# Kernel tuning notes

Measured on AMD Instinct MI355X. Metric: run time of the kernel, lower is better.

Reference implementation:

```python
import jax, jax.numpy as jnp
import numpy as np

D_MODEL = 1024
NUM_HEADS = 16
D_K = D_MODEL // NUM_HEADS
THETA = 10000.0


def _rope(x, pos):
    # x: [B, H, S, D_K], pos: [S]
    angles = 1.0 / (THETA ** (jnp.arange(0, D_K, 2, dtype=jnp.float32) / D_K))  # [D_K/2]
    ang = pos.astype(jnp.float32)[:, None] * angles  # [S, D_K/2]
    cos = jnp.repeat(jnp.cos(ang), 2, axis=-1)  # [S, D_K]
    sin = jnp.repeat(jnp.sin(ang), 2, axis=-1)
    x2 = x.reshape(*x.shape[:-1], D_K // 2, 2)
    xr = jnp.stack([-x2[..., 1], x2[..., 0]], axis=-1).reshape(x.shape)
    return x * cos + xr * sin


def setup_inputs() -> dict:
    key = jax.random.key(0)
    ks = jax.random.split(key, 5)
    B, S = 2, 2048
    sd = np.sqrt(2.0 / (D_MODEL + D_MODEL))
    return {
        "x": jax.random.normal(ks[0], (B, S, D_MODEL), dtype=jnp.float32),
        "token_positions": jnp.arange(S, dtype=jnp.int32),
        "Wq": jax.random.normal(ks[1], (D_MODEL, D_MODEL), dtype=jnp.float32) * sd,
        "Wk": jax.random.normal(ks[2], (D_MODEL, D_MODEL), dtype=jnp.float32) * sd,
        "Wv": jax.random.normal(ks[3], (D_MODEL, D_MODEL), dtype=jnp.float32) * sd,
        "Wo": jax.random.normal(ks[4], (D_MODEL, D_MODEL), dtype=jnp.float32) * sd,
    }


def reference(x, token_positions, Wq, Wk, Wv, Wo):
    B, S, _ = x.shape

    def proj_heads(W):
        y = jnp.einsum('bsd,ed->bse', x, W)  # weight stored [d_out, d_in]
        return y.reshape(B, S, NUM_HEADS, D_K).transpose(0, 2, 1, 3)  # [B,H,S,Dk]

    q = _rope(proj_heads(Wq), token_positions)
    k = _rope(proj_heads(Wk), token_positions)
    v = proj_heads(Wv)

    scores = jnp.einsum('bhqd,bhkd->bhqk', q, k) / np.sqrt(D_K)  # [B,H,S,S]
    causal = jnp.tril(jnp.ones((S, S), dtype=bool))
    scores = jnp.where(causal, scores, -jnp.inf)
    attn = jax.nn.softmax(scores, axis=-1)
    out = jnp.einsum('bhqk,bhkd->bhqd', attn, v)  # [B,H,S,Dk]
    out = out.transpose(0, 2, 1, 3).reshape(B, S, D_MODEL)
    return jnp.einsum('bsd,ed->bse', out, Wo)
```

## Files before the change

### kernel.cpp

```cpp
#include <hip/hip_runtime.h>
#include <hip/hip_bf16.h>
#include <cstdint>
#include <cmath>

#define SEQ 2048
#define NH 16
#define DM 1024
#define BATCH 2

typedef short bf16x8 __attribute__((ext_vector_type(8)));
typedef float f32x4 __attribute__((ext_vector_type(4)));
typedef const void __attribute__((address_space(1)))* gas_t;
typedef void __attribute__((address_space(3)))* las_t;

#if __has_builtin(__builtin_amdgcn_exp2f)
#define EXP2(x) __builtin_amdgcn_exp2f(x)
#else
#define EXP2(x) __expf((x) * 0.6931471805599453f)
#endif

#define QSCALE 0.18033688011112042f

static __device__ __forceinline__ unsigned short f2bf(float f) {
    union { __hip_bfloat16 h; unsigned short u; } cv;
    cv.h = __float2bfloat16(f);
    return cv.u;
}
static __device__ __forceinline__ float bf2f(unsigned short u) {
    union { unsigned short u; __hip_bfloat16 h; } cv;
    cv.u = u;
    return __bfloat162float(cv.h);
}

static __device__ __forceinline__ void gload_lds16(const void* g, void* l) {
    __builtin_amdgcn_global_load_lds(
        reinterpret_cast<gas_t>(reinterpret_cast<uintptr_t>(g)),
        reinterpret_cast<las_t>(reinterpret_cast<uintptr_t>(l)),
        16, 0, 0);
}

__global__ __launch_bounds__(256) void cvt_all(
    const float* __restrict__ x,  const float* __restrict__ wq,
    const float* __restrict__ wk, const float* __restrict__ wv,
    const float* __restrict__ wo,
    unsigned short* __restrict__ xb, unsigned short* __restrict__ wqkv,
    unsigned short* __restrict__ wob) {
    int blk = blockIdx.x;
    const float* src; unsigned short* dst; int base;
    if (blk < 4096)      { src = x;  dst = xb;              base = blk; }
    else if (blk < 5120) { src = wq; dst = wqkv;            base = blk - 4096; }
    else if (blk < 6144) { src = wk; dst = wqkv + 1048576;  base = blk - 5120; }
    else if (blk < 7168) { src = wv; dst = wqkv + 2097152;  base = blk - 6144; }
    else                 { src = wo; dst = wob;             base = blk - 7168; }
    int i = base * 256 + threadIdx.x;
    float4 v = reinterpret_cast<const float4*>(src)[i];
    ushort4 o;
    o.x = f2bf(v.x); o.y = f2bf(v.y); o.z = f2bf(v.z); o.w = f2bf(v.w);
    reinterpret_cast<ushort4*>(dst)[i] = o;
}

template<int OUT_BF16>
__global__ __launch_bounds__(256) void gemm_bt(
    const unsigned short* __restrict__ A,
    const unsigned short* __restrict__ B,
    void* __restrict__ C, int M, int N, int K) {
    __shared__ unsigned short As[128 * 32];
    __shared__ unsigned short Bs[128 * 32];
    const int tid = threadIdx.x;
    const int lane = tid & 63, wid = tid >> 6;
    const int wr = wid >> 1, wc = wid & 1;
    const int ln15 = lane & 15, kq = lane >> 4;
    const int bm = blockIdx.y, bn = blockIdx.x;

    f32x4 acc[4][4] = {};
    const int nk = K >> 5;
    for (int kt = 0; kt < nk; ++kt) {
        #pragma unroll
        for (int i = 0; i < 2; ++i) {
            int c = i * 256 + tid;
            int row = c >> 2, k8 = (c & 3) << 3;
            size_t gofsA = (size_t)(bm * 128 + row) * K + kt * 32 + k8;
            size_t gofsB = (size_t)(bn * 128 + row) * K + kt * 32 + k8;
            unsigned ldsoff = (unsigned)(i * 256 + wid * 64) * 16;
            gload_lds16(A + gofsA, (char*)As + ldsoff);
            gload_lds16(B + gofsB, (char*)Bs + ldsoff);
        }
        __syncthreads();
        bf16x8 af[4], bf[4];
        #pragma unroll
        for (int m = 0; m < 4; ++m)
            af[m] = *reinterpret_cast<const bf16x8*>(&As[(wr * 64 + m * 16 + ln15) * 32 + kq * 8]);
        #pragma unroll
        for (int n = 0; n < 4; ++n)
            bf[n] = *reinterpret_cast<const bf16x8*>(&Bs[(wc * 64 + n * 16 + ln15) * 32 + kq * 8]);
        #pragma unroll
        for (int m = 0; m < 4; ++m)
            #pragma unroll
            for (int n = 0; n < 4; ++n)
                acc[m][n] = __builtin_amdgcn_mfma_f32_16x16x32_bf16(af[m], bf[n], acc[m][n], 0, 0, 0);
        __syncthreads();
    }
    #pragma unroll
    for (int m = 0; m < 4; ++m) {
        #pragma unroll
        for (int n = 0; n < 4; ++n) {
            int col = bn * 128 + wc * 64 + n * 16 + ln15;
            #pragma unroll
            for (int j = 0; j < 4; ++j) {
                int row = bm * 128 + wr * 64 + m * 16 + kq * 4 + j;
                if constexpr (OUT_BF16 != 0)
                    ((unsigned short*)C)[(size_t)row * N + col] = f2bf(acc[m][n][j]);
                else
                    ((float*)C)[(size_t)row * N + col] = acc[m][n][j];
            }
        }
    }
}

__global__ __launch_bounds__(512) void gemm256_bt(
    const unsigned short* __restrict__ A,
    const unsigned short* __restrict__ B,
    unsigned short* __restrict__ C, int M, int N, int K) {
    __shared__ unsigned short As[2][256 * 64];
    __shared__ unsigned short Bs[2][256 * 64];
    const int tid = threadIdx.x;
    const int lane = tid & 63, wid = tid >> 6;
    const int wm = wid >> 2, wn = wid & 3;
    const int ln15 = lane & 15, g = lane >> 4;
    const int bm = blockIdx.y, bn = blockIdx.x;

    const unsigned short* aSrc[4];
    const unsigned short* bSrc[4];
    #pragma unroll
    for (int p = 0; p < 4; ++p) {
        int c = tid + (p << 9);
        int row = c >> 3, slot = c & 7;
        aSrc[p] = A + (size_t)(bm * 256 + row) * K + ((slot ^ (row & 7)) << 3);
        bSrc[p] = B + (size_t)(bn * 256 + row) * K + ((slot ^ (row & 7)) << 3);
    }
    auto stage = [&](int kt, int buf) {
        #pragma unroll
        for (int p = 0; p < 4; ++p) {
            unsigned dst = (unsigned)(tid + (p << 9)) << 4;
            gload_lds16(aSrc[p] + kt * 64, (char*)As[buf] + dst);
            gload_lds16(bSrc[p] + kt * 64, (char*)Bs[buf] + dst);
        }
    };

    const unsigned ps0 = (unsigned)((g ^ (ln15 & 7)) << 4);
    const unsigned ps1 = (unsigned)(((4 + g) ^ (ln15 & 7)) << 4);
    const unsigned aBase = (unsigned)(wm * 128 + ln15) * 128;
    const unsigned bBase = (unsigned)(wn * 64 + ln15) * 128;

    f32x4 acc[8][4] = {};
    const int nkt = K >> 6;

    stage(0, 0);
    stage(1, 1);

    for (int t = 0; t < nkt; ++t) {
        const int cur = t & 1;
        if (t + 1 < nkt) {
            asm volatile("s_waitcnt vmcnt(8)" ::: "memory");
        } else {
            asm volatile("s_waitcnt vmcnt(0)" ::: "memory");
        }
        __builtin_amdgcn_s_barrier();

        const char* Ab = (const char*)As[cur];
        const char* Bb = (const char*)Bs[cur];
        bf16x8 bf[4][2];
        #pragma unroll
        for (int nf = 0; nf < 4; ++nf) {
            bf[nf][0] = *reinterpret_cast<const bf16x8*>(Bb + bBase + nf * 2048 + ps0);
            bf[nf][1] = *reinterpret_cast<const bf16x8*>(Bb + bBase + nf * 2048 + ps1);
        }
        __builtin_amdgcn_s_setprio(1);
        #pragma unroll
        for (int mf = 0; mf < 8; ++mf) {
            bf16x8 af0 = *reinterpret_cast<const bf16x8*>(Ab + aBase + mf * 2048 + ps0);
            bf16x8 af1 = *reinterpret_cast<const bf16x8*>(Ab + aBase + mf * 2048 + ps1);
            #pragma unroll
            for (int nf = 0; nf < 4; ++nf) {
                acc[mf][nf] = __builtin_amdgcn_mfma_f32_16x16x32_bf16(af0, bf[nf][0], acc[mf][nf], 0, 0, 0);
                acc[mf][nf] = __builtin_amdgcn_mfma_f32_16x16x32_bf16(af1, bf[nf][1], acc[mf][nf], 0, 0, 0);
            }
        }
        __builtin_amdgcn_s_setprio(0);
        asm volatile("s_waitcnt lgkmcnt(0)" ::: "memory");
        __builtin_amdgcn_s_barrier();
        if (t + 2 < nkt) stage(t + 2, cur);
    }

    #pragma unroll
    for (int mf = 0; mf < 8; ++mf) {
        #pragma unroll
        for (int nf = 0; nf < 4; ++nf) {
            int col = bn * 256 + wn * 64 + nf * 16 + ln15;
            #pragma unroll
            for (int j = 0; j < 4; ++j) {
                int row = bm * 256 + wm * 128 + mf * 16 + g * 4 + j;
                C[(size_t)row * N + col] = f2bf(acc[mf][nf][j]);
            }
        }
    }
}

__global__ __launch_bounds__(256) void rope_table(const int* __restrict__ pos,
                                                  float2* __restrict__ tab) {
    int idx = blockIdx.x * 256 + threadIdx.x;
    int s = idx >> 5, i = idx & 31;
    float fpos = (float)pos[s];
    float freq = exp2f(-(float)i * (13.287712379549449f / 32.0f));
    float ang = fpos * freq, sn, cs;
    sincosf(ang, &sn, &cs);
    tab[idx] = make_float2(cs, sn);
}

__global__ __launch_bounds__(256) void rope_kernel(
    const unsigned short* __restrict__ qkv, const float2* __restrict__ tab,
    unsigned short* __restrict__ Qh, unsigned short* __restrict__ Kh) {
    int bs = blockIdx.x;
    int b = bs >> 11, s = bs & (SEQ - 1);
    int t = threadIdx.x;
    #pragma unroll
    for (int p = t; p < 512; p += 256) {
        int h = p >> 5, i = p & 31;
        float2 cs = tab[(s << 5) + i];
        size_t src = (size_t)bs * 3072 + h * 64 + 2 * i;
        size_t dst = ((size_t)(b * NH + h) * SEQ + s) * 64 + 2 * i;
        ushort2 qv = *reinterpret_cast<const ushort2*>(qkv + src);
        float q0 = bf2f(qv.x), q1 = bf2f(qv.y);
        ushort2 qo;
        qo.x = f2bf((q0 * cs.x - q1 * cs.y) * QSCALE);
        qo.y = f2bf((q1 * cs.x + q0 * cs.y) * QSCALE);
        *reinterpret_cast<ushort2*>(Qh + dst) = qo;
        ushort2 kv = *reinterpret_cast<const ushort2*>(qkv + src + 1024);
        float k0 = bf2f(kv.x), k1 = bf2f(kv.y);
        ushort2 ko;
        ko.x = f2bf(k0 * cs.x - k1 * cs.y);
        ko.y = f2bf(k1 * cs.x + k0 * cs.y);
        *reinterpret_cast<ushort2*>(Kh + dst) = ko;
    }
}

__global__ __launch_bounds__(256) void vtrans_kernel(
    const unsigned short* __restrict__ qkv, unsigned short* __restrict__ Vo) {
    __shared__ unsigned short tile[64][65];
    int blk = blockIdx.x;
    int st = blk & 31, bh = blk >> 5;
    int sb = st * 64;
    int t = threadIdx.x;
    int b = bh >> 4, h = bh & 15;
    #pragma unroll
    for (int u = t; u < 1024; u += 256) {
        int sl = u >> 4, d4 = (u & 15) << 2;
        ushort4 v = *reinterpret_cast<const ushort4*>(
            qkv + (size_t)(b * SEQ + sb + sl) * 3072 + 2048 + h * 64 + d4);
        tile[sl][d4] = v.x; tile[sl][d4 + 1] = v.y;
        tile[sl][d4 + 2] = v.z; tile[sl][d4 + 3] = v.w;
    }
    __syncthreads();
    #pragma unroll
    for (int u = t; u < 1024; u += 256) {
        int d = u >> 4, s4 = (u & 15) << 2;
        ushort4 o;
        o.x = tile[s4][d]; o.y = tile[s4 + 1][d];
        o.z = tile[s4 + 2][d]; o.w = tile[s4 + 3][d];
        *reinterpret_cast<ushort4*>(Vo + ((size_t)bh * 64 + d) * SEQ + sb + s4) = o;
    }
}

__global__ __launch_bounds__(128) void attn_kernel(
    const unsigned short* __restrict__ Qh, const unsigned short* __restrict__ Kh,
    const unsigned short* __restrict__ Vt, unsigned short* __restrict__ Out) {
    __shared__ unsigned short Kb[2][64 * 64];
    __shared__ unsigned short Vb[2][64 * 64];
    __shared__ unsigned short Plds[2][16 * 72];

    const int tid = threadIdx.x;
    const int wid = tid >> 6, lane = tid & 63;
    const int ln15 = lane & 15, g = lane >> 4;
    const int bid = blockIdx.x;
    const int bh = bid & 31;
    const int pb = bid >> 5;

    const unsigned short* Qp = Qh + (size_t)bh * SEQ * 64;
    const unsigned short* Kp = Kh + (size_t)bh * SEQ * 64;
    const unsigned short* Vp = Vt + (size_t)bh * 64 * SEQ;
    char* Pc = (char*)Plds[wid];

    const unsigned short* kSrc[4];
    const unsigned short* vSrc[4];
    #pragma unroll
    for (int p = 0; p < 4; ++p) {
        int c = tid + (p << 7);
        int row = c >> 3, slot = c & 7;
        kSrc[p] = Kp + (size_t)row * 64 + ((slot ^ (row & 7)) << 3);
        vSrc[p] = Vp + (size_t)row * SEQ + ((slot ^ (row & 7)) << 3);
    }

    auto stage = [&](int kb, int buf) {
        #pragma unroll
        for (int p = 0; p < 4; ++p) {
            unsigned bb = (unsigned)(wid * 1024 + p * 2048);
            gload_lds16(kSrc[p] + (size_t)kb * 64, (char*)Kb[buf] + bb);
            gload_lds16(vSrc[p] + kb, (char*)Vb[buf] + bb);
        }
    };

    unsigned kOff[4][2], vOff[4][2];
    #pragma unroll
    for (int s = 0; s < 4; ++s) {
        int r = ln15 + 16 * s;
        kOff[s][0] = r * 128 + ((g ^ (r & 7)) << 4);
        kOff[s][1] = r * 128 + (((4 + g) ^ (r & 7)) << 4);
    }
    #pragma unroll
    for (int c = 0; c < 4; ++c) {
        int d = c * 16 + ln15;
        vOff[c][0] = d * 128 + ((g ^ (d & 7)) << 4);
        vOff[c][1] = d * 128 + (((4 + g) ^ (d & 7)) << 4);
    }
    const unsigned pW = (unsigned)(ln15 * 144 + 8 * g);
    const unsigned pR = (unsigned)(ln15 * 144 + 16 * g);

    const int b = bh >> 4, h = bh & 15;

    for (int bi = 0; bi < 2; ++bi) {
        const int bnd = bi ? (63 - pb) : pb;
        const int qb = bnd * 32 + wid * 16;
        const int nt = (bnd + 2) >> 1;
        const int thr = qb + ln15 - 4 * g;

        bf16x8 aq0 = *reinterpret_cast<const bf16x8*>(Qp + (size_t)(qb + ln15) * 64 + g * 8);
        bf16x8 aq1 = *reinterpret_cast<const bf16x8*>(Qp + (size_t)(qb + ln15) * 64 + 32 + g * 8);

        f32x4 oacc[4] = {};
        float lsum = 0.f;

        stage(0, 0);

        for (int t = 0; t < nt; ++t) {
            const int kb = t << 6;
            const int cur = t & 1;
            if (t + 1 < nt) {
                stage((t + 1) << 6, cur ^ 1);
                asm volatile("s_waitcnt vmcnt(8)" ::: "memory");
            } else {
                asm volatile("s_waitcnt vmcnt(0)" ::: "memory");
            }
            __builtin_amdgcn_s_barrier();

            const char* K0 = (const char*)Kb[cur];
            const char* V0 = (const char*)Vb[cur];
            bf16x8 kf[8], bv[8];
            #pragma unroll
            for (int s = 0; s < 4; ++s) {
                kf[2 * s]     = *reinterpret_cast<const bf16x8*>(K0 + kOff[s][0]);
                kf[2 * s + 1] = *reinterpret_cast<const bf16x8*>(K0 + kOff[s][1]);
            }
            #pragma unroll
            for (int c = 0; c < 4; ++c) {
                bv[2 * c]     = *reinterpret_cast<const bf16x8*>(V0 + vOff[c][0]);
                bv[2 * c + 1] = *reinterpret_cast<const bf16x8*>(V0 + vOff[c][1]);
            }

            const f32x4 z = {};
            f32x4 sq[4];
            #pragma unroll
            for (int s = 0; s < 4; ++s) {
                sq[s] = __builtin_amdgcn_mfma_f32_16x16x32_bf16(kf[2 * s], aq0, z, 0, 0, 0);
                sq[s] = __builtin_amdgcn_mfma_f32_16x16x32_bf16(kf[2 * s + 1], aq1, sq[s], 0, 0, 0);
            }

            float pv[4][4];
            if (t == nt - 1) {
                #pragma unroll
                for (int s = 0; s < 4; ++s)
                    #pragma unroll
                    for (int j = 0; j < 4; ++j)
                        pv[s][j] = (j <= thr - kb - 16 * s) ? EXP2(sq[s][j]) : 0.f;
            } else {
                #pragma unroll
                for (int s = 0; s < 4; ++s)
                    #pragma unroll
                    for (int j = 0; j < 4; ++j)
                        pv[s][j] = EXP2(sq[s][j]);
            }
            #pragma unroll
            for (int s = 0; s < 4; ++s)
                lsum += (pv[s][0] + pv[s][1]) + (pv[s][2] + pv[s][3]);

            #pragma unroll
            for (int s = 0; s < 4; ++s) {
                ushort4 w;
                w.x = f2bf(pv[s][0]); w.y = f2bf(pv[s][1]);
                w.z = f2bf(pv[s][2]); w.w = f2bf(pv[s][3]);
                *reinterpret_cast<ushort4*>(Pc + pW + 32 * s) = w;
            }
            asm volatile("s_waitcnt lgkmcnt(0)" ::: "memory");
            bf16x8 ap0 = *reinterpret_cast<const bf16x8*>(Pc + pR);
            bf16x8 ap1 = *reinterpret_cast<const bf16x8*>(Pc + pR + 64);
            #pragma unroll
            for (int c = 0; c < 4; ++c) {
                oacc[c] = __builtin_amdgcn_mfma_f32_16x16x32_bf16(ap0, bv[2 * c], oacc[c], 0, 0, 0);
                oacc[c] = __builtin_amdgcn_mfma_f32_16x16x32_bf16(ap1, bv[2 * c + 1], oacc[c], 0, 0, 0);
            }
            asm volatile("s_waitcnt lgkmcnt(0)" ::: "memory");
            __builtin_amdgcn_s_barrier();
        }

        float r = lsum;
        r += __shfl_xor(r, 16);
        r += __shfl_xor(r, 32);
        float linv = 1.f / r;
        float invj[4];
        #pragma unroll
        for (int j = 0; j < 4; ++j)
            invj[j] = __shfl(linv, 20 * g + j);
        #pragma unroll
        for (int c = 0; c < 4; ++c)
            #pragma unroll
            for (int j = 0; j < 4; ++j) {
                int s = qb + g * 4 + j;
                Out[((size_t)(b * SEQ + s)) * DM + h * 64 + c * 16 + ln15] =
                    f2bf(oacc[c][j] * invj[j]);
            }
    }
}

extern "C" void kernel_launch(void* const* d_in, const int* in_sizes, int n_in,
                              void* d_out, int out_size, void* d_ws, size_t ws_size,
                              hipStream_t stream) {
    const float* x = (const float*)d_in[0];
    const int* pos = (const int*)d_in[1];
    const float* Wq = (const float*)d_in[2];
    const float* Wk = (const float*)d_in[3];
    const float* Wv = (const float*)d_in[4];
    const float* Wo = (const float*)d_in[5];
    float* out = (float*)d_out;

    char* ws = (char*)d_ws;
    const size_t MB = 1024 * 1024;
    unsigned short* xb   = (unsigned short*)(ws + 0 * MB);
    unsigned short* wqkv = (unsigned short*)(ws + 8 * MB);
    unsigned short* wob  = (unsigned short*)(ws + 14 * MB);
    unsigned short* qkv  = (unsigned short*)(ws + 16 * MB);
    float2*         tab  = (float2*)       (ws + 40 * MB);
    unsigned short* qh   = (unsigned short*)(ws + 41 * MB);
    unsigned short* kh   = (unsigned short*)(ws + 49 * MB);
    unsigned short* vtr  = (unsigned short*)(ws + 57 * MB);
    unsigned short* att  = (unsigned short*)(ws + 65 * MB);

    cvt_all<<<8192, 256, 0, stream>>>(x, Wq, Wk, Wv, Wo, xb, wqkv, wob);
    rope_table<<<256, 256, 0, stream>>>(pos, tab);

    gemm256_bt<<<dim3(12, 16), 512, 0, stream>>>(xb, wqkv, qkv, 4096, 3072, 1024);

    rope_kernel<<<4096, 256, 0, stream>>>(qkv, tab, qh, kh);
    vtrans_kernel<<<1024, 256, 0, stream>>>(qkv, vtr);

    attn_kernel<<<1024, 128, 0, stream>>>(qh, kh, vtr, att);

    gemm_bt<0><<<dim3(8, 32), 256, 0, stream>>>(att, wob, out, 4096, 1024, 1024);
}
```

Baseline: 126.8 us.

## Interleave half-tile global-to-LDS loads with MFMA clusters in GEMM main loop

Restructures the 256x256 bf16 GEMM main loop into an 8-wave-style ping-pong schedule. Each k-tile's compute is split into four MFMA clusters. A and B loads for upcoming tiles are issued in half-tile pieces between those clusters, with barriers around each cluster. The aim is finer overlap of global-to-LDS traffic with matrix math than the old stage-whole-tile-then-compute loop. In exchange it adds more barriers per k-tile and more delicate buffer-reuse ordering, since A for the next tile is written into a buffer while other waves may still read the current one.

Result: faster. 124.1 us (-2.1%).

```diff
diff --git a/kernel.cpp b/kernel.cpp
--- a/kernel.cpp
+++ b/kernel.cpp
@@ -138,12 +138,18 @@
         aSrc[p] = A + (size_t)(bm * 256 + row) * K + ((slot ^ (row & 7)) << 3);
         bSrc[p] = B + (size_t)(bn * 256 + row) * K + ((slot ^ (row & 7)) << 3);
     }
-    auto stage = [&](int kt, int buf) {
-        #pragma unroll
-        for (int p = 0; p < 4; ++p) {
+    auto stageA = [&](int kt, int h) {
+        #pragma unroll
+        for (int p = 2 * h; p < 2 * h + 2; ++p) {
             unsigned dst = (unsigned)(tid + (p << 9)) << 4;
-            gload_lds16(aSrc[p] + kt * 64, (char*)As[buf] + dst);
-            gload_lds16(bSrc[p] + kt * 64, (char*)Bs[buf] + dst);
+            gload_lds16(aSrc[p] + kt * 64, (char*)As[kt & 1] + dst);
+        }
+    };
+    auto stageB = [&](int kt, int h) {
+        #pragma unroll
+        for (int p = 2 * h; p < 2 * h + 2; ++p) {
+            unsigned dst = (unsigned)(tid + (p << 9)) << 4;
+            gload_lds16(bSrc[p] + kt * 64, (char*)Bs[kt & 1] + dst);
         }
     };
 
@@ -154,42 +160,70 @@
 
     f32x4 acc[8][4] = {};
     const int nkt = K >> 6;
-
-    stage(0, 0);
-    stage(1, 1);
-
-    for (int t = 0; t < nkt; ++t) {
-        const int cur = t & 1;
-        if (t + 1 < nkt) {
-            asm volatile("s_waitcnt vmcnt(8)" ::: "memory");
-        } else {
-            asm volatile("s_waitcnt vmcnt(0)" ::: "memory");
-        }
-        __builtin_amdgcn_s_barrier();
-
-        const char* Ab = (const char*)As[cur];
-        const char* Bb = (const char*)Bs[cur];
-        bf16x8 bf[4][2];
-        #pragma unroll
-        for (int nf = 0; nf < 4; ++nf) {
-            bf[nf][0] = *reinterpret_cast<const bf16x8*>(Bb + bBase + nf * 2048 + ps0);
-            bf[nf][1] = *reinterpret_cast<const bf16x8*>(Bb + bBase + nf * 2048 + ps1);
-        }
-        __builtin_amdgcn_s_setprio(1);
-        #pragma unroll
-        for (int mf = 0; mf < 8; ++mf) {
-            bf16x8 af0 = *reinterpret_cast<const bf16x8*>(Ab + aBase + mf * 2048 + ps0);
-            bf16x8 af1 = *reinterpret_cast<const bf16x8*>(Ab + aBase + mf * 2048 + ps1);
-            #pragma unroll
-            for (int nf = 0; nf < 4; ++nf) {
-                acc[mf][nf] = __builtin_amdgcn_mfma_f32_16x16x32_bf16(af0, bf[nf][0], acc[mf][nf], 0, 0, 0);
-                acc[mf][nf] = __builtin_amdgcn_mfma_f32_16x16x32_bf16(af1, bf[nf][1], acc[mf][nf], 0, 0, 0);
-            }
-        }
-        __builtin_amdgcn_s_setprio(0);
-        asm volatile("s_waitcnt lgkmcnt(0)" ::: "memory");
-        __builtin_amdgcn_s_barrier();
-        if (t + 2 < nkt) stage(t + 2, cur);
+    const int nit = nkt >> 1;
+
+    stageA(0, 0); stageA(0, 1);
+    stageB(0, 0); stageB(0, 1);
+    stageB(1, 0); stageB(1, 1);
+    asm volatile("s_waitcnt vmcnt(0)" ::: "memory");
+    __builtin_amdgcn_s_barrier();
+
+    for (int j = 0; j < nit; ++j) {
+        const int t0 = 2 * j, t1 = 2 * j + 1;
+        const bool more = (t0 + 2) < nkt;
+        #pragma unroll
+        for (int grp = 0; grp < 2; ++grp) {
+            const char* Ab = (const char*)As[grp];
+            const char* Bb = (const char*)Bs[grp];
+            bf16x8 bfr[4][2];
+            #pragma unroll
+            for (int q = 0; q < 4; ++q) {
+                if (q == 0) {
+                    #pragma unroll
+                    for (int nf = 0; nf < 4; ++nf) {
+                        bfr[nf][0] = *reinterpret_cast<const bf16x8*>(Bb + bBase + nf * 2048 + ps0);
+                        bfr[nf][1] = *reinterpret_cast<const bf16x8*>(Bb + bBase + nf * 2048 + ps1);
+                    }
+                }
+                bf16x8 af0 = *reinterpret_cast<const bf16x8*>(Ab + aBase + (2 * q) * 2048 + ps0);
+                bf16x8 af1 = *reinterpret_cast<const bf16x8*>(Ab + aBase + (2 * q) * 2048 + ps1);
+                bf16x8 af2 = *reinterpret_cast<const bf16x8*>(Ab + aBase + (2 * q + 1) * 2048 + ps0);
+                bf16x8 af3 = *reinterpret_cast<const bf16x8*>(Ab + aBase + (2 * q + 1) * 2048 + ps1);
+
+                if (grp == 0) {
+                    if (q == 0) stageA(t1, 0);
+                    else if (q == 1) stageA(t1, 1);
+                    else if (q == 2) { if (more) stageB(t0 + 2, 0); }
+                    else {
+                        if (more) { stageB(t0 + 2, 1);
+                                    asm volatile("s_waitcnt vmcnt(4)" ::: "memory"); }
+                        else      { asm volatile("s_waitcnt vmcnt(0)" ::: "memory"); }
+                    }
+                } else {
+                    if (q == 0)      { if (more) stageA(t0 + 2, 0); }
+                    else if (q == 1) { if (more) stageA(t0 + 2, 1); }
+                    else if (q == 2) { if (more) stageB(t1 + 2, 0); }
+                    else {
+                        if (more) { stageB(t1 + 2, 1);
+                                    asm volatile("s_waitcnt vmcnt(4)" ::: "memory"); }
+                        else      { asm volatile("s_waitcnt vmcnt(0)" ::: "memory"); }
+                    }
+                }
+
+                __builtin_amdgcn_s_barrier();
+                asm volatile("s_waitcnt lgkmcnt(0)" ::: "memory");
+                __builtin_amdgcn_s_setprio(1);
+                #pragma unroll
+                for (int nf = 0; nf < 4; ++nf) {
+                    acc[2 * q][nf] = __builtin_amdgcn_mfma_f32_16x16x32_bf16(af0, bfr[nf][0], acc[2 * q][nf], 0, 0, 0);
+                    acc[2 * q][nf] = __builtin_amdgcn_mfma_f32_16x16x32_bf16(af1, bfr[nf][1], acc[2 * q][nf], 0, 0, 0);
+                    acc[2 * q + 1][nf] = __builtin_amdgcn_mfma_f32_16x16x32_bf16(af2, bfr[nf][0], acc[2 * q + 1][nf], 0, 0, 0);
+                    acc[2 * q + 1][nf] = __builtin_amdgcn_mfma_f32_16x16x32_bf16(af3, bfr[nf][1], acc[2 * q + 1][nf], 0, 0, 0);
+                }
+                __builtin_amdgcn_s_setprio(0);
+                __builtin_amdgcn_s_barrier();
+            }
+        }
     }
 
     #pragma unroll
```
